# Kernel optimization log

Hardware: AMD Instinct MI355X
Metric: run time of the kernel (lower is better)

## Reference

```python
import jax, jax.numpy as jnp
import numpy as np

N_HEADS = 16
ROPE_BASE = 10000.0


def _rope_cos_sin(seq_len, head_dim, dtype):
    half = head_dim // 2
    inv_freq = 1.0 / (ROPE_BASE ** (jnp.arange(0, half, dtype=jnp.float32) / half))
    ang = jnp.arange(seq_len, dtype=jnp.float32)[:, None] * inv_freq[None, :]  # [S, half]
    cos = jnp.concatenate([jnp.cos(ang), jnp.cos(ang)], axis=-1).astype(dtype)  # [S, hd]
    sin = jnp.concatenate([jnp.sin(ang), jnp.sin(ang)], axis=-1).astype(dtype)
    return cos, sin


def _rotate_half(x):
    half = x.shape[-1] // 2
    return jnp.concatenate([-x[..., half:], x[..., :half]], axis=-1)


def setup_inputs() -> dict:
    key = jax.random.key(0)
    k1, k2, k3 = jax.random.split(key, 3)
    B, S, D = 2, 2048, 1024
    x = jax.random.normal(k1, (B, S, D), dtype=jnp.float32)
    w_qkv = jax.random.normal(k2, (D, 3 * D), dtype=jnp.float32) * (1.0 / np.sqrt(D))
    w_out = jax.random.normal(k3, (D, D), dtype=jnp.float32) * (1.0 / np.sqrt(D))
    return {"x": x, "w_qkv": w_qkv, "w_out": w_out}


def reference(x, w_qkv, w_out):
    B, S, D = x.shape
    H = N_HEADS
    hd = D // H
    scale = 1.0 / np.sqrt(hd)

    qkv = x @ w_qkv  # [B, S, 3D]
    q, k, v = jnp.split(qkv, 3, axis=-1)
    # [B, H, S, hd]
    q = q.reshape(B, S, H, hd).transpose(0, 2, 1, 3)
    k = k.reshape(B, S, H, hd).transpose(0, 2, 1, 3)
    v = v.reshape(B, S, H, hd).transpose(0, 2, 1, 3)

    cos, sin = _rope_cos_sin(S, hd, x.dtype)  # [S, hd]
    q = q * cos + _rotate_half(q) * sin
    k = k * cos + _rotate_half(k) * sin

    scores = jnp.einsum("bhqd,bhkd->bhqk", q, k) * scale  # [B, H, S, S]
    causal = jnp.tril(jnp.ones((S, S), dtype=bool))
    scores = jnp.where(causal[None, None, :, :], scores, -jnp.inf)

    probs = jax.nn.softmax(scores.astype(jnp.float32), axis=-1).astype(q.dtype)
    out = jnp.einsum("bhqk,bhkd->bhqd", probs, v)  # [B, H, S, hd]
    out = out.transpose(0, 2, 1, 3).reshape(B, S, D)
    return out @ w_out
```

## Files before the change

kernel.cpp:

```cpp
#include <hip/hip_runtime.h>
#include <math.h>
#include <type_traits>

#define B_  2
#define S_  2048
#define D_  1024
#define H_  16

typedef short bf16x8 __attribute__((ext_vector_type(8)));
typedef float f32x4  __attribute__((ext_vector_type(4)));

__device__ __forceinline__ short f2bf(float f) {
    unsigned u = __builtin_bit_cast(unsigned, f);
    u += 0x7FFFu + ((u >> 16) & 1u);
    return (short)(u >> 16);
}
__device__ __forceinline__ float bf2f(short s) {
    unsigned u = ((unsigned)(unsigned short)s) << 16;
    return __builtin_bit_cast(float, u);
}

__device__ __forceinline__ void gload16(const short* g, const void* l) {
    __builtin_amdgcn_global_load_lds(
        (const __attribute__((address_space(1))) void*)g,
        (__attribute__((address_space(3))) void*)l, 16, 0, 0);
}

__global__ __launch_bounds__(256) void cvt_bf16_kernel(
    const float* __restrict__ in, short* __restrict__ out)
{
    int i = (blockIdx.x * 256 + threadIdx.x) * 8;
    float4 a = *(const float4*)(in + i);
    float4 b = *(const float4*)(in + i + 4);
    bf16x8 o;
    o[0] = f2bf(a.x); o[1] = f2bf(a.y); o[2] = f2bf(a.z); o[3] = f2bf(a.w);
    o[4] = f2bf(b.x); o[5] = f2bf(b.y); o[6] = f2bf(b.z); o[7] = f2bf(b.w);
    *(bf16x8*)(out + i) = o;
}

__global__ __launch_bounds__(256) void transpose_cvt_kernel(
    const float* __restrict__ in, short* __restrict__ out, int K, int N)
{
    __shared__ short t[64][72];
    const int k0 = blockIdx.y * 64, n0 = blockIdx.x * 64;
    const int r = threadIdx.x >> 2;
    const int c = (threadIdx.x & 3) * 16;
    const float* src = in + (size_t)(k0 + r) * N + n0 + c;
#pragma unroll
    for (int i = 0; i < 16; ++i) t[c + i][r] = f2bf(src[i]);
    __syncthreads();
    short* dst = out + (size_t)(n0 + r) * K + k0 + c;
    *(bf16x8*)(dst)     = *(const bf16x8*)&t[r][c];
    *(bf16x8*)(dst + 8) = *(const bf16x8*)&t[r][c + 8];
}

__global__ __launch_bounds__(256) void rope_tab_kernel(float2* __restrict__ tab)
{
    int idx = blockIdx.x * 256 + threadIdx.x;
    int j = idx & 31, s = idx >> 5;
    float inv = powf(10000.0f, -(float)j * (1.0f / 32.0f));
    float sn, cs;
    sincosf((float)s * inv, &sn, &cs);
    tab[idx] = make_float2(cs, sn);
}

template <typename OutT>
__global__ __launch_bounds__(256) void gemm_bt(
    const short* __restrict__ A, const short* __restrict__ Bt,
    OutT* __restrict__ C, int M, int N, int K)
{
    __shared__ short As[128 * 32];
    __shared__ short Bs[128 * 32];

    const int tid  = threadIdx.x;
    const int wave = tid >> 6, lane = tid & 63;
    const int quad = lane >> 4, l16 = lane & 15;
    const int wm = wave >> 1, wn = wave & 1;
    const int row0 = blockIdx.y * 128, col0 = blockIdx.x * 128;

    f32x4 acc[4][4];
#pragma unroll
    for (int mi = 0; mi < 4; ++mi)
#pragma unroll
        for (int ni = 0; ni < 4; ++ni) acc[mi][ni] = (f32x4)0.f;

    const int sr = tid >> 2;
    const int sc = (tid & 3) * 8;
    const short* a0 = A  + (size_t)(row0 + sr) * K + sc;
    const short* a1 = A  + (size_t)(row0 + 64 + sr) * K + sc;
    const short* b0 = Bt + (size_t)(col0 + sr) * K + sc;
    const short* b1 = Bt + (size_t)(col0 + 64 + sr) * K + sc;
    char* lA0 = (char*)As + wave * 1024;
    char* lA1 = (char*)As + 4096 + wave * 1024;
    char* lB0 = (char*)Bs + wave * 1024;
    char* lB1 = (char*)Bs + 4096 + wave * 1024;

    for (int k0 = 0; k0 < K; k0 += 32) {
        __syncthreads();
        gload16(a0 + k0, lA0);
        gload16(a1 + k0, lA1);
        gload16(b0 + k0, lB0);
        gload16(b1 + k0, lB1);
        __syncthreads();

        bf16x8 af[4], bfr[4];
#pragma unroll
        for (int mi = 0; mi < 4; ++mi)
            af[mi] = *(const bf16x8*)(As + (wm * 64 + mi * 16 + l16) * 32 + quad * 8);
#pragma unroll
        for (int ni = 0; ni < 4; ++ni)
            bfr[ni] = *(const bf16x8*)(Bs + (wn * 64 + ni * 16 + l16) * 32 + quad * 8);
#pragma unroll
        for (int mi = 0; mi < 4; ++mi)
#pragma unroll
            for (int ni = 0; ni < 4; ++ni)
                acc[mi][ni] = __builtin_amdgcn_mfma_f32_16x16x32_bf16(
                    af[mi], bfr[ni], acc[mi][ni], 0, 0, 0);
    }

#pragma unroll
    for (int mi = 0; mi < 4; ++mi) {
#pragma unroll
        for (int ni = 0; ni < 4; ++ni) {
#pragma unroll
            for (int r = 0; r < 4; ++r) {
                int row = row0 + wm * 64 + mi * 16 + quad * 4 + r;
                int col = col0 + wn * 64 + ni * 16 + l16;
                float v = acc[mi][ni][r];
                if constexpr (std::is_same_v<OutT, short>)
                    C[(size_t)row * N + col] = f2bf(v);
                else
                    C[(size_t)row * N + col] = v;
            }
        }
    }
}

__global__ __launch_bounds__(256) void convert_kernel(
    const short* __restrict__ qkvb, const float2* __restrict__ tab,
    short* __restrict__ Qb, short* __restrict__ Kb, short* __restrict__ Vt)
{
    __shared__ short vtile[64][72];
    const int bh = blockIdx.y;
    const int st = blockIdx.x;
    const int b = bh >> 4, h = bh & 15;

    const int sl = threadIdx.x >> 2;
    const int g  = threadIdx.x & 3;
    const int s  = st * 64 + sl;
    const short* row = qkvb + (size_t)(b * S_ + s) * 3072 + h * 64;

    const int j0 = g * 8;
    bf16x8 q1v = *(const bf16x8*)(row + j0);
    bf16x8 q2v = *(const bf16x8*)(row + 32 + j0);
    bf16x8 k1v = *(const bf16x8*)(row + 1024 + j0);
    bf16x8 k2v = *(const bf16x8*)(row + 1056 + j0);
    bf16x8 qlo, qhi, klo, khi;
#pragma unroll
    for (int i = 0; i < 8; ++i) {
        float2 t = tab[s * 32 + j0 + i];
        float q1 = bf2f(q1v[i]), q2 = bf2f(q2v[i]);
        float k1 = bf2f(k1v[i]), k2 = bf2f(k2v[i]);
        qlo[i] = f2bf((q1 * t.x - q2 * t.y) * 0.125f);
        qhi[i] = f2bf((q2 * t.x + q1 * t.y) * 0.125f);
        klo[i] = f2bf(k1 * t.x - k2 * t.y);
        khi[i] = f2bf(k2 * t.x + k1 * t.y);
    }
    size_t oq = ((size_t)bh * S_ + s) * 64;
    *(bf16x8*)(Qb + oq + j0)      = qlo;
    *(bf16x8*)(Qb + oq + 32 + j0) = qhi;
    size_t ok = ((size_t)bh * S_ + s) * 72;
    *(bf16x8*)(Kb + ok + j0)      = klo;
    *(bf16x8*)(Kb + ok + 32 + j0) = khi;

    bf16x8 v0 = *(const bf16x8*)(row + 2048 + g * 16);
    bf16x8 v1 = *(const bf16x8*)(row + 2048 + g * 16 + 8);
#pragma unroll
    for (int i = 0; i < 8; ++i) {
        vtile[g * 16 + i][sl]     = v0[i];
        vtile[g * 16 + 8 + i][sl] = v1[i];
    }
    __syncthreads();
    size_t vo = ((size_t)bh * 64 + sl) * S_ + st * 64 + g * 16;
    *(bf16x8*)(Vt + vo)     = *(const bf16x8*)&vtile[sl][g * 16];
    *(bf16x8*)(Vt + vo + 8) = *(const bf16x8*)&vtile[sl][g * 16 + 8];
}

__global__ __launch_bounds__(256) void attn_kernel(
    const short* __restrict__ Qb, const short* __restrict__ Kb,
    const short* __restrict__ Vt, short* __restrict__ Opart,
    float* __restrict__ lpart)
{
    __shared__ short Ks[2][64 * 72];
    __shared__ short Vs[2][64 * 72];
    __shared__ short Ps[64][72];

    const int lin = blockIdx.x;
    const int xcd = lin & 7;
    const int j   = lin >> 3;
    const int bh   = xcd * 4 + (j & 3);
    const int task = j >> 2;

    const int g = task < 8 ? 0 : task < 24 ? 1 : task < 48 ? 2 : 3;
    const int cumstart = g == 0 ? 0 : g == 1 ? 8 : g == 2 ? 24 : 48;
    const int idx = task - cumstart;
    const int qd = idx / (g + 1);
    const int qb = 8 * g + qd;
    const int c  = idx - qd * (g + 1);
    const int t0 = c * 8;
    const int t1 = min(qb, c * 8 + 7);

    const int wave = threadIdx.x >> 6, lane = threadIdx.x & 63;
    const int quad = lane >> 4, l16 = lane & 15;
    const size_t head64 = (size_t)bh * S_ * 64;
    const size_t headK  = (size_t)bh * S_ * 72;

    const short* qrow = Qb + head64
        + (size_t)(qb * 64 + wave * 16 + l16) * 64 + quad * 8;
    const bf16x8 qf0 = *(const bf16x8*)(qrow);
    const bf16x8 qf1 = *(const bf16x8*)(qrow + 32);

    bf16x8 ones;
#pragma unroll
    for (int i = 0; i < 8; ++i) ones[i] = (short)0x3F80;

    int vr[3], vc[3];
#pragma unroll
    for (int u = 0; u < 3; ++u) {
        int jj = wave + u * 4;
        int e = jj * 64 + lane;
        vr[u] = e / 9;
        vc[u] = e * 8 - vr[u] * 72;
    }

    auto stageKV = [&](int buf, int t) {
        const short* kt  = Kb + headK + (size_t)t * 4608;
        const short* vtb = Vt + head64 + t * 64;
        short* kl = Ks[buf];
        short* vl = Vs[buf];
#pragma unroll
        for (int u = 0; u < 3; ++u) {
            int jj = wave + u * 4;
            if (jj < 9) {
                gload16(kt + jj * 512 + lane * 8, (char*)kl + jj * 1024);
                gload16(vtb + (size_t)vr[u] * S_ + vc[u], (char*)vl + jj * 1024);
            }
        }
    };

    f32x4 lacc = (f32x4)0.f;
    f32x4 oacc[4];
#pragma unroll
    for (int nt = 0; nt < 4; ++nt) oacc[nt] = (f32x4)0.f;

    int buf = 0;
    stageKV(0, t0);
    for (int t = t0; t <= t1; ++t) {
        __syncthreads();
        if (t < t1) stageKV(buf ^ 1, t + 1);

        const short* kb = Ks[buf];
        const short* vb = Vs[buf];

        f32x4 s4[4];
#pragma unroll
        for (int nt = 0; nt < 4; ++nt) {
            const short* kr = kb + (nt * 16 + l16) * 72 + quad * 8;
            bf16x8 b0 = *(const bf16x8*)kr;
            bf16x8 b1 = *(const bf16x8*)(kr + 32);
            f32x4 a = (f32x4)0.f;
            a = __builtin_amdgcn_mfma_f32_16x16x32_bf16(qf0, b0, a, 0, 0, 0);
            a = __builtin_amdgcn_mfma_f32_16x16x32_bf16(qf1, b1, a, 0, 0, 0);
            s4[nt] = a;
        }

        if (t == qb) {
#pragma unroll
            for (int nt = 0; nt < 4; ++nt)
#pragma unroll
                for (int r = 0; r < 4; ++r)
                    if (nt * 16 + l16 > wave * 16 + quad * 4 + r)
                        s4[nt][r] = -INFINITY;
        }

#pragma unroll
        for (int nt = 0; nt < 4; ++nt)
#pragma unroll
            for (int r = 0; r < 4; ++r)
                Ps[wave * 16 + quad * 4 + r][nt * 16 + l16] =
                    f2bf(__expf(s4[nt][r] - 8.0f));

        bf16x8 pa0 = *(const bf16x8*)&Ps[wave * 16 + l16][quad * 8];
        bf16x8 pa1 = *(const bf16x8*)&Ps[wave * 16 + l16][32 + quad * 8];
        lacc = __builtin_amdgcn_mfma_f32_16x16x32_bf16(pa0, ones, lacc, 0, 0, 0);
        lacc = __builtin_amdgcn_mfma_f32_16x16x32_bf16(pa1, ones, lacc, 0, 0, 0);
#pragma unroll
        for (int nt = 0; nt < 4; ++nt) {
            const short* vrp = vb + (nt * 16 + l16) * 72 + quad * 8;
            bf16x8 vb0 = *(const bf16x8*)vrp;
            bf16x8 vb1 = *(const bf16x8*)(vrp + 32);
            oacc[nt] = __builtin_amdgcn_mfma_f32_16x16x32_bf16(
                pa0, vb0, oacc[nt], 0, 0, 0);
            oacc[nt] = __builtin_amdgcn_mfma_f32_16x16x32_bf16(
                pa1, vb1, oacc[nt], 0, 0, 0);
        }
        buf ^= 1;
    }

    const int pidx = bh * 80 + task;
#pragma unroll
    for (int r = 0; r < 4; ++r) {
        int ql = wave * 16 + quad * 4 + r;
        short* orow = Opart + (size_t)pidx * 4096 + ql * 64;
#pragma unroll
        for (int nt = 0; nt < 4; ++nt)
            orow[nt * 16 + l16] = f2bf(oacc[nt][r]);
        if (l16 == 0)
            lpart[(size_t)pidx * 64 + ql] = lacc[r];
    }
}

__global__ __launch_bounds__(256) void combine_kernel(
    const short* __restrict__ Opart, const float* __restrict__ lpart,
    short* __restrict__ attnb)
{
    const int qb = blockIdx.x, bh = blockIdx.y;
    const int g = qb >> 3, nch = g + 1;
    const int cbase = bh * 80 + nch * (qb - 4 * g);
    const int q = threadIdx.x >> 2;
    const int dg = (threadIdx.x & 3) * 16;

    float lsum = 0.f;
    float acc[16];
#pragma unroll
    for (int i = 0; i < 16; ++i) acc[i] = 0.f;

    for (int cc = 0; cc < nch; ++cc) {
        lsum += lpart[(size_t)(cbase + cc) * 64 + q];
        const short* src = Opart + (size_t)(cbase + cc) * 4096 + q * 64 + dg;
        bf16x8 o0 = *(const bf16x8*)src;
        bf16x8 o1 = *(const bf16x8*)(src + 8);
#pragma unroll
        for (int i = 0; i < 8; ++i) {
            acc[i]     += bf2f(o0[i]);
            acc[i + 8] += bf2f(o1[i]);
        }
    }
    float inv = 1.0f / lsum;
    const int b = bh >> 4, h = bh & 15;
    bf16x8 r0, r1;
#pragma unroll
    for (int i = 0; i < 8; ++i) {
        r0[i] = f2bf(acc[i] * inv);
        r1[i] = f2bf(acc[i + 8] * inv);
    }
    short* dst = attnb + (size_t)(b * S_ + qb * 64 + q) * 1024 + h * 64 + dg;
    *(bf16x8*)dst       = r0;
    *(bf16x8*)(dst + 8) = r1;
}

extern "C" void kernel_launch(void* const* d_in, const int* in_sizes, int n_in,
                              void* d_out, int out_size, void* d_ws, size_t ws_size,
                              hipStream_t stream)
{
    const float* x     = (const float*)d_in[0];
    const float* w_qkv = (const float*)d_in[1];
    const float* w_out = (const float*)d_in[2];
    float* out = (float*)d_out;

    short* qkvb = (short*)d_ws;
    short* Qb   = qkvb + (size_t)4096 * 3072;
    short* Kb   = Qb   + (size_t)4096 * 1024;
    short* Vt   = Kb   + (size_t)32 * 2048 * 72;
    short* Xb   = Vt   + (size_t)4096 * 1024;
    short* Wqt  = Xb   + (size_t)4096 * 1024;
    short* Wot  = Wqt  + (size_t)3072 * 1024;
    float2* tab = (float2*)(Wot + (size_t)1024 * 1024);
    short* Opart = qkvb;
    float* lbuf  = (float*)Wqt;
    short* attnb = Xb;

    cvt_bf16_kernel<<<(4096 * 1024 / 8) / 256, 256, 0, stream>>>(x, Xb);
    transpose_cvt_kernel<<<dim3(3072 / 64, 1024 / 64), 256, 0, stream>>>(
        w_qkv, Wqt, 1024, 3072);
    transpose_cvt_kernel<<<dim3(1024 / 64, 1024 / 64), 256, 0, stream>>>(
        w_out, Wot, 1024, 1024);
    rope_tab_kernel<<<(2048 * 32) / 256, 256, 0, stream>>>(tab);

    gemm_bt<short><<<dim3(3072 / 128, 4096 / 128), 256, 0, stream>>>(
        Xb, Wqt, qkvb, 4096, 3072, 1024);

    convert_kernel<<<dim3(S_ / 64, B_ * H_), 256, 0, stream>>>(qkvb, tab, Qb, Kb, Vt);

    attn_kernel<<<2560, 256, 0, stream>>>(Qb, Kb, Vt, Opart, lbuf);

    combine_kernel<<<dim3(32, 32), 256, 0, stream>>>(Opart, lbuf, attnb);

    gemm_bt<float><<<dim3(1024 / 128, 4096 / 128), 256, 0, stream>>>(
        attnb, Wot, out, 4096, 1024, 1024);
}
```

Baseline: 210.7 us.

## Double attention query tile to 128 rows per block for K/V reuse

Each attention block now handles 128 query rows (two 16-row MFMA subtiles per wave) instead of 64, so every staged K/V tile in LDS feeds twice as many MFMAs. The grid halves to 1280 blocks, the split-KV task map is rebuilt for 128-row query tiles, the causal mask uses absolute positions, and combine_kernel reads the new partial layout. This cuts global K/V traffic and LDS staging per unit of work, at the cost of more registers, a larger LDS P buffer, fewer blocks, and some wasted masked work on diagonal tiles.

```diff
diff --git a/kernel.cpp b/kernel.cpp
--- a/kernel.cpp
+++ b/kernel.cpp
@@ -193,32 +193,34 @@
 {
     __shared__ short Ks[2][64 * 72];
     __shared__ short Vs[2][64 * 72];
-    __shared__ short Ps[64][72];
+    __shared__ short Ps[128][72];
 
     const int lin = blockIdx.x;
     const int xcd = lin & 7;
-    const int j   = lin >> 3;
-    const int bh   = xcd * 4 + (j & 3);
-    const int task = j >> 2;
-
-    const int g = task < 8 ? 0 : task < 24 ? 1 : task < 48 ? 2 : 3;
-    const int cumstart = g == 0 ? 0 : g == 1 ? 8 : g == 2 ? 24 : 48;
-    const int idx = task - cumstart;
-    const int qd = idx / (g + 1);
-    const int qb = 8 * g + qd;
-    const int c  = idx - qd * (g + 1);
+    const int bh   = xcd * 4 + ((lin >> 3) & 3);
+    const int task = lin >> 5;
+
+    const int g = task < 4 ? 0 : task < 12 ? 1 : task < 24 ? 2 : 3;
+    const int cum = g == 0 ? 0 : g == 1 ? 4 : g == 2 ? 12 : 24;
+    const int idx = task - cum;
+    const int qt = 4 * g + idx / (g + 1);
+    const int c  = idx % (g + 1);
     const int t0 = c * 8;
-    const int t1 = min(qb, c * 8 + 7);
+    const int t1 = min(2 * qt + 1, c * 8 + 7);
 
     const int wave = threadIdx.x >> 6, lane = threadIdx.x & 63;
     const int quad = lane >> 4, l16 = lane & 15;
     const size_t head64 = (size_t)bh * S_ * 64;
     const size_t headK  = (size_t)bh * S_ * 72;
 
-    const short* qrow = Qb + head64
-        + (size_t)(qb * 64 + wave * 16 + l16) * 64 + quad * 8;
-    const bf16x8 qf0 = *(const bf16x8*)(qrow);
-    const bf16x8 qf1 = *(const bf16x8*)(qrow + 32);
+    bf16x8 qf[2][2];
+#pragma unroll
+    for (int mi = 0; mi < 2; ++mi) {
+        const short* qrow = Qb + head64
+            + (size_t)(qt * 128 + wave * 32 + mi * 16 + l16) * 64 + quad * 8;
+        qf[mi][0] = *(const bf16x8*)(qrow);
+        qf[mi][1] = *(const bf16x8*)(qrow + 32);
+    }
 
     bf16x8 ones;
 #pragma unroll
@@ -248,10 +250,14 @@
         }
     };
 
-    f32x4 lacc = (f32x4)0.f;
-    f32x4 oacc[4];
-#pragma unroll
-    for (int nt = 0; nt < 4; ++nt) oacc[nt] = (f32x4)0.f;
+    f32x4 lacc[2];
+    f32x4 oacc[2][4];
+#pragma unroll
+    for (int mi = 0; mi < 2; ++mi) {
+        lacc[mi] = (f32x4)0.f;
+#pragma unroll
+        for (int nt = 0; nt < 4; ++nt) oacc[mi][nt] = (f32x4)0.f;
+    }
 
     int buf = 0;
     stageKV(0, t0);
@@ -262,62 +268,81 @@
         const short* kb = Ks[buf];
         const short* vb = Vs[buf];
 
-        f32x4 s4[4];
+        f32x4 s4[2][4];
 #pragma unroll
         for (int nt = 0; nt < 4; ++nt) {
             const short* kr = kb + (nt * 16 + l16) * 72 + quad * 8;
             bf16x8 b0 = *(const bf16x8*)kr;
             bf16x8 b1 = *(const bf16x8*)(kr + 32);
-            f32x4 a = (f32x4)0.f;
-            a = __builtin_amdgcn_mfma_f32_16x16x32_bf16(qf0, b0, a, 0, 0, 0);
-            a = __builtin_amdgcn_mfma_f32_16x16x32_bf16(qf1, b1, a, 0, 0, 0);
-            s4[nt] = a;
-        }
-
-        if (t == qb) {
+#pragma unroll
+            for (int mi = 0; mi < 2; ++mi) {
+                f32x4 a = (f32x4)0.f;
+                a = __builtin_amdgcn_mfma_f32_16x16x32_bf16(qf[mi][0], b0, a, 0, 0, 0);
+                a = __builtin_amdgcn_mfma_f32_16x16x32_bf16(qf[mi][1], b1, a, 0, 0, 0);
+                s4[mi][nt] = a;
+            }
+        }
+
+        if (t >= 2 * qt) {
+            const int kbase = t * 64;
+            const int qbase = qt * 128 + wave * 32 + quad * 4;
+#pragma unroll
+            for (int mi = 0; mi < 2; ++mi)
+#pragma unroll
+                for (int nt = 0; nt < 4; ++nt)
+#pragma unroll
+                    for (int r = 0; r < 4; ++r)
+                        if (kbase + nt * 16 + l16 > qbase + mi * 16 + r)
+                            s4[mi][nt][r] = -INFINITY;
+        }
+
+#pragma unroll
+        for (int mi = 0; mi < 2; ++mi)
 #pragma unroll
             for (int nt = 0; nt < 4; ++nt)
 #pragma unroll
                 for (int r = 0; r < 4; ++r)
-                    if (nt * 16 + l16 > wave * 16 + quad * 4 + r)
-                        s4[nt][r] = -INFINITY;
-        }
-
-#pragma unroll
-        for (int nt = 0; nt < 4; ++nt)
-#pragma unroll
-            for (int r = 0; r < 4; ++r)
-                Ps[wave * 16 + quad * 4 + r][nt * 16 + l16] =
-                    f2bf(__expf(s4[nt][r] - 8.0f));
-
-        bf16x8 pa0 = *(const bf16x8*)&Ps[wave * 16 + l16][quad * 8];
-        bf16x8 pa1 = *(const bf16x8*)&Ps[wave * 16 + l16][32 + quad * 8];
-        lacc = __builtin_amdgcn_mfma_f32_16x16x32_bf16(pa0, ones, lacc, 0, 0, 0);
-        lacc = __builtin_amdgcn_mfma_f32_16x16x32_bf16(pa1, ones, lacc, 0, 0, 0);
+                    Ps[wave * 32 + mi * 16 + quad * 4 + r][nt * 16 + l16] =
+                        f2bf(__expf(s4[mi][nt][r] - 8.0f));
+
+        bf16x8 vfr[4][2];
 #pragma unroll
         for (int nt = 0; nt < 4; ++nt) {
             const short* vrp = vb + (nt * 16 + l16) * 72 + quad * 8;
-            bf16x8 vb0 = *(const bf16x8*)vrp;
-            bf16x8 vb1 = *(const bf16x8*)(vrp + 32);
-            oacc[nt] = __builtin_amdgcn_mfma_f32_16x16x32_bf16(
-                pa0, vb0, oacc[nt], 0, 0, 0);
-            oacc[nt] = __builtin_amdgcn_mfma_f32_16x16x32_bf16(
-                pa1, vb1, oacc[nt], 0, 0, 0);
+            vfr[nt][0] = *(const bf16x8*)vrp;
+            vfr[nt][1] = *(const bf16x8*)(vrp + 32);
+        }
+
+#pragma unroll
+        for (int mi = 0; mi < 2; ++mi) {
+            bf16x8 pa0 = *(const bf16x8*)&Ps[wave * 32 + mi * 16 + l16][quad * 8];
+            bf16x8 pa1 = *(const bf16x8*)&Ps[wave * 32 + mi * 16 + l16][32 + quad * 8];
+            lacc[mi] = __builtin_amdgcn_mfma_f32_16x16x32_bf16(pa0, ones, lacc[mi], 0, 0, 0);
+            lacc[mi] = __builtin_amdgcn_mfma_f32_16x16x32_bf16(pa1, ones, lacc[mi], 0, 0, 0);
+#pragma unroll
+            for (int nt = 0; nt < 4; ++nt) {
+                oacc[mi][nt] = __builtin_amdgcn_mfma_f32_16x16x32_bf16(
+                    pa0, vfr[nt][0], oacc[mi][nt], 0, 0, 0);
+                oacc[mi][nt] = __builtin_amdgcn_mfma_f32_16x16x32_bf16(
+                    pa1, vfr[nt][1], oacc[mi][nt], 0, 0, 0);
+            }
         }
         buf ^= 1;
     }
 
-    const int pidx = bh * 80 + task;
-#pragma unroll
-    for (int r = 0; r < 4; ++r) {
-        int ql = wave * 16 + quad * 4 + r;
-        short* orow = Opart + (size_t)pidx * 4096 + ql * 64;
-#pragma unroll
-        for (int nt = 0; nt < 4; ++nt)
-            orow[nt * 16 + l16] = f2bf(oacc[nt][r]);
-        if (l16 == 0)
-            lpart[(size_t)pidx * 64 + ql] = lacc[r];
-    }
+    const int pidx = bh * 40 + task;
+#pragma unroll
+    for (int mi = 0; mi < 2; ++mi)
+#pragma unroll
+        for (int r = 0; r < 4; ++r) {
+            int ql = wave * 32 + mi * 16 + quad * 4 + r;
+            short* orow = Opart + (size_t)pidx * 8192 + ql * 64;
+#pragma unroll
+            for (int nt = 0; nt < 4; ++nt)
+                orow[nt * 16 + l16] = f2bf(oacc[mi][nt][r]);
+            if (l16 == 0)
+                lpart[(size_t)pidx * 128 + ql] = lacc[mi][r];
+        }
 }
 
 __global__ __launch_bounds__(256) void combine_kernel(
@@ -325,10 +350,15 @@
     short* __restrict__ attnb)
 {
     const int qb = blockIdx.x, bh = blockIdx.y;
-    const int g = qb >> 3, nch = g + 1;
-    const int cbase = bh * 80 + nch * (qb - 4 * g);
+    const int qt = qb >> 1;
+    const int g = qt < 4 ? 0 : qt < 8 ? 1 : qt < 12 ? 2 : 3;
+    const int tb = (g == 0 ? 0 : g == 1 ? 4 : g == 2 ? 12 : 24)
+                   + (qt - 4 * g) * (g + 1);
+    const int nch = g + 1;
+    const int cbase = bh * 40 + tb;
     const int q = threadIdx.x >> 2;
     const int dg = (threadIdx.x & 3) * 16;
+    const int qrow = (qb & 1) * 64 + q;
 
     float lsum = 0.f;
     float acc[16];
@@ -336,8 +366,8 @@
     for (int i = 0; i < 16; ++i) acc[i] = 0.f;
 
     for (int cc = 0; cc < nch; ++cc) {
-        lsum += lpart[(size_t)(cbase + cc) * 64 + q];
-        const short* src = Opart + (size_t)(cbase + cc) * 4096 + q * 64 + dg;
+        lsum += lpart[(size_t)(cbase + cc) * 128 + qrow];
+        const short* src = Opart + (size_t)(cbase + cc) * 8192 + qrow * 64 + dg;
         bf16x8 o0 = *(const bf16x8*)src;
         bf16x8 o1 = *(const bf16x8*)(src + 8);
 #pragma unroll
@@ -392,7 +422,7 @@
 
     convert_kernel<<<dim3(S_ / 64, B_ * H_), 256, 0, stream>>>(qkvb, tab, Qb, Kb, Vt);
 
-    attn_kernel<<<2560, 256, 0, stream>>>(Qb, Kb, Vt, Opart, lbuf);
+    attn_kernel<<<1280, 256, 0, stream>>>(Qb, Kb, Vt, Opart, lbuf);
 
     combine_kernel<<<dim3(32, 32), 256, 0, stream>>>(Opart, lbuf, attnb);
 
```

After: 209.8 us. Within noise of the previous version (-0.4%).

## Fuse RoPE, scaling and V transpose into QKV GEMM epilogue

Applied to the files above, without the earlier changes.

The separate convert kernel is removed. The QKV GEMM epilogue now applies RoPE and the Q scale and writes Q/K in head-major layout, and it writes V transposed directly. This saves the round trip of the bf16 qkv intermediate through global memory and one kernel launch. In exchange, the epilogue stores are scalar 2-byte writes, or 8-byte writes for V, with strided addresses. The workspace is re-laid out so Opart and lbuf no longer alias the old qkv buffer.

```diff
diff --git a/kernel.cpp b/kernel.cpp
--- a/kernel.cpp
+++ b/kernel.cpp
@@ -8,6 +8,7 @@
 #define H_  16
 
 typedef short bf16x8 __attribute__((ext_vector_type(8)));
+typedef short bf16x4 __attribute__((ext_vector_type(4)));
 typedef float f32x4  __attribute__((ext_vector_type(4)));
 
 __device__ __forceinline__ short f2bf(float f) {
@@ -64,10 +65,9 @@
     tab[idx] = make_float2(cs, sn);
 }
 
-template <typename OutT>
-__global__ __launch_bounds__(256) void gemm_bt(
+__global__ __launch_bounds__(256) void gemm_bt_f32(
     const short* __restrict__ A, const short* __restrict__ Bt,
-    OutT* __restrict__ C, int M, int N, int K)
+    float* __restrict__ C, int M, int N, int K)
 {
     __shared__ short As[128 * 32];
     __shared__ short Bs[128 * 32];
@@ -119,71 +119,121 @@
     }
 
 #pragma unroll
-    for (int mi = 0; mi < 4; ++mi) {
-#pragma unroll
-        for (int ni = 0; ni < 4; ++ni) {
+    for (int mi = 0; mi < 4; ++mi)
+#pragma unroll
+        for (int ni = 0; ni < 4; ++ni)
 #pragma unroll
             for (int r = 0; r < 4; ++r) {
                 int row = row0 + wm * 64 + mi * 16 + quad * 4 + r;
                 int col = col0 + wn * 64 + ni * 16 + l16;
-                float v = acc[mi][ni][r];
-                if constexpr (std::is_same_v<OutT, short>)
-                    C[(size_t)row * N + col] = f2bf(v);
-                else
-                    C[(size_t)row * N + col] = v;
+                C[(size_t)row * N + col] = acc[mi][ni][r];
             }
-        }
-    }
-}
-
-__global__ __launch_bounds__(256) void convert_kernel(
-    const short* __restrict__ qkvb, const float2* __restrict__ tab,
+}
+
+__global__ __launch_bounds__(256) void gemm_qkv(
+    const short* __restrict__ A, const short* __restrict__ Bt,
+    const float2* __restrict__ tab,
     short* __restrict__ Qb, short* __restrict__ Kb, short* __restrict__ Vt)
 {
-    __shared__ short vtile[64][72];
-    const int bh = blockIdx.y;
-    const int st = blockIdx.x;
-    const int b = bh >> 4, h = bh & 15;
-
-    const int sl = threadIdx.x >> 2;
-    const int g  = threadIdx.x & 3;
-    const int s  = st * 64 + sl;
-    const short* row = qkvb + (size_t)(b * S_ + s) * 3072 + h * 64;
-
-    const int j0 = g * 8;
-    bf16x8 q1v = *(const bf16x8*)(row + j0);
-    bf16x8 q2v = *(const bf16x8*)(row + 32 + j0);
-    bf16x8 k1v = *(const bf16x8*)(row + 1024 + j0);
-    bf16x8 k2v = *(const bf16x8*)(row + 1056 + j0);
-    bf16x8 qlo, qhi, klo, khi;
-#pragma unroll
-    for (int i = 0; i < 8; ++i) {
-        float2 t = tab[s * 32 + j0 + i];
-        float q1 = bf2f(q1v[i]), q2 = bf2f(q2v[i]);
-        float k1 = bf2f(k1v[i]), k2 = bf2f(k2v[i]);
-        qlo[i] = f2bf((q1 * t.x - q2 * t.y) * 0.125f);
-        qhi[i] = f2bf((q2 * t.x + q1 * t.y) * 0.125f);
-        klo[i] = f2bf(k1 * t.x - k2 * t.y);
-        khi[i] = f2bf(k2 * t.x + k1 * t.y);
-    }
-    size_t oq = ((size_t)bh * S_ + s) * 64;
-    *(bf16x8*)(Qb + oq + j0)      = qlo;
-    *(bf16x8*)(Qb + oq + 32 + j0) = qhi;
-    size_t ok = ((size_t)bh * S_ + s) * 72;
-    *(bf16x8*)(Kb + ok + j0)      = klo;
-    *(bf16x8*)(Kb + ok + 32 + j0) = khi;
-
-    bf16x8 v0 = *(const bf16x8*)(row + 2048 + g * 16);
-    bf16x8 v1 = *(const bf16x8*)(row + 2048 + g * 16 + 8);
-#pragma unroll
-    for (int i = 0; i < 8; ++i) {
-        vtile[g * 16 + i][sl]     = v0[i];
-        vtile[g * 16 + 8 + i][sl] = v1[i];
-    }
-    __syncthreads();
-    size_t vo = ((size_t)bh * 64 + sl) * S_ + st * 64 + g * 16;
-    *(bf16x8*)(Vt + vo)     = *(const bf16x8*)&vtile[sl][g * 16];
-    *(bf16x8*)(Vt + vo + 8) = *(const bf16x8*)&vtile[sl][g * 16 + 8];
+    const int K = 1024;
+    __shared__ short As[128 * 32];
+    __shared__ short Bs[128 * 32];
+
+    const int tid  = threadIdx.x;
+    const int wave = tid >> 6, lane = tid & 63;
+    const int quad = lane >> 4, l16 = lane & 15;
+    const int wm = wave >> 1, wn = wave & 1;
+    const int row0 = blockIdx.y * 128, col0 = blockIdx.x * 128;
+
+    f32x4 acc[4][4];
+#pragma unroll
+    for (int mi = 0; mi < 4; ++mi)
+#pragma unroll
+        for (int ni = 0; ni < 4; ++ni) acc[mi][ni] = (f32x4)0.f;
+
+    const int sr = tid >> 2;
+    const int sc = (tid & 3) * 8;
+    const short* a0 = A  + (size_t)(row0 + sr) * K + sc;
+    const short* a1 = A  + (size_t)(row0 + 64 + sr) * K + sc;
+    const short* b0 = Bt + (size_t)(col0 + sr) * K + sc;
+    const short* b1 = Bt + (size_t)(col0 + 64 + sr) * K + sc;
+    char* lA0 = (char*)As + wave * 1024;
+    char* lA1 = (char*)As + 4096 + wave * 1024;
+    char* lB0 = (char*)Bs + wave * 1024;
+    char* lB1 = (char*)Bs + 4096 + wave * 1024;
+
+    for (int k0 = 0; k0 < K; k0 += 32) {
+        __syncthreads();
+        gload16(a0 + k0, lA0);
+        gload16(a1 + k0, lA1);
+        gload16(b0 + k0, lB0);
+        gload16(b1 + k0, lB1);
+        __syncthreads();
+
+        bf16x8 af[4], bfr[4];
+#pragma unroll
+        for (int mi = 0; mi < 4; ++mi)
+            af[mi] = *(const bf16x8*)(As + (wm * 64 + mi * 16 + l16) * 32 + quad * 8);
+#pragma unroll
+        for (int ni = 0; ni < 4; ++ni)
+            bfr[ni] = *(const bf16x8*)(Bs + (wn * 64 + ni * 16 + l16) * 32 + quad * 8);
+#pragma unroll
+        for (int mi = 0; mi < 4; ++mi)
+#pragma unroll
+            for (int ni = 0; ni < 4; ++ni)
+                acc[mi][ni] = __builtin_amdgcn_mfma_f32_16x16x32_bf16(
+                    af[mi], bfr[ni], acc[mi][ni], 0, 0, 0);
+    }
+
+    const int sec  = (col0 + wn * 64) >> 6;
+    const int h    = sec & 15;
+    const int kind = sec >> 4;
+
+    if (kind < 2) {
+#pragma unroll
+        for (int mi = 0; mi < 4; ++mi) {
+#pragma unroll
+            for (int r = 0; r < 4; ++r) {
+                int row = row0 + wm * 64 + mi * 16 + quad * 4 + r;
+                int b = row >> 11, s = row & (S_ - 1);
+                int bh = b * 16 + h;
+#pragma unroll
+                for (int ni = 0; ni < 2; ++ni) {
+                    int j = ni * 16 + l16;
+                    float2 t = tab[s * 32 + j];
+                    float lo = acc[mi][ni][r], hi = acc[mi][ni + 2][r];
+                    float olo = lo * t.x - hi * t.y;
+                    float ohi = hi * t.x + lo * t.y;
+                    if (kind == 0) {
+                        size_t base = ((size_t)bh * S_ + s) * 64;
+                        Qb[base + j]      = f2bf(olo * 0.125f);
+                        Qb[base + 32 + j] = f2bf(ohi * 0.125f);
+                    } else {
+                        size_t base = ((size_t)bh * S_ + s) * 72;
+                        Kb[base + j]      = f2bf(olo);
+                        Kb[base + 32 + j] = f2bf(ohi);
+                    }
+                }
+            }
+        }
+    } else {
+#pragma unroll
+        for (int mi = 0; mi < 4; ++mi) {
+            int srow0 = row0 + wm * 64 + mi * 16 + quad * 4;
+            int b = srow0 >> 11, s0 = srow0 & (S_ - 1);
+            int bh = b * 16 + h;
+#pragma unroll
+            for (int ni = 0; ni < 4; ++ni) {
+                int d = ni * 16 + l16;
+                bf16x4 p;
+                p[0] = f2bf(acc[mi][ni][0]);
+                p[1] = f2bf(acc[mi][ni][1]);
+                p[2] = f2bf(acc[mi][ni][2]);
+                p[3] = f2bf(acc[mi][ni][3]);
+                *(bf16x4*)(Vt + ((size_t)bh * 64 + d) * S_ + s0) = p;
+            }
+        }
+    }
 }
 
 __global__ __launch_bounds__(256) void attn_kernel(
@@ -368,16 +418,15 @@
     const float* w_out = (const float*)d_in[2];
     float* out = (float*)d_out;
 
-    short* qkvb = (short*)d_ws;
-    short* Qb   = qkvb + (size_t)4096 * 3072;
+    short* Qb   = (short*)d_ws;
     short* Kb   = Qb   + (size_t)4096 * 1024;
     short* Vt   = Kb   + (size_t)32 * 2048 * 72;
     short* Xb   = Vt   + (size_t)4096 * 1024;
     short* Wqt  = Xb   + (size_t)4096 * 1024;
     short* Wot  = Wqt  + (size_t)3072 * 1024;
     float2* tab = (float2*)(Wot + (size_t)1024 * 1024);
-    short* Opart = qkvb;
-    float* lbuf  = (float*)Wqt;
+    short* Opart = (short*)(tab + 2048 * 32);
+    float* lbuf  = (float*)(Opart + (size_t)2560 * 4096);
     short* attnb = Xb;
 
     cvt_bf16_kernel<<<(4096 * 1024 / 8) / 256, 256, 0, stream>>>(x, Xb);
@@ -387,15 +436,13 @@
         w_out, Wot, 1024, 1024);
     rope_tab_kernel<<<(2048 * 32) / 256, 256, 0, stream>>>(tab);
 
-    gemm_bt<short><<<dim3(3072 / 128, 4096 / 128), 256, 0, stream>>>(
-        Xb, Wqt, qkvb, 4096, 3072, 1024);
-
-    convert_kernel<<<dim3(S_ / 64, B_ * H_), 256, 0, stream>>>(qkvb, tab, Qb, Kb, Vt);
+    gemm_qkv<<<dim3(3072 / 128, 4096 / 128), 256, 0, stream>>>(
+        Xb, Wqt, tab, Qb, Kb, Vt);
 
     attn_kernel<<<2560, 256, 0, stream>>>(Qb, Kb, Vt, Opart, lbuf);
 
     combine_kernel<<<dim3(32, 32), 256, 0, stream>>>(Opart, lbuf, attnb);
 
-    gemm_bt<float><<<dim3(1024 / 128, 4096 / 128), 256, 0, stream>>>(
+    gemm_bt_f32<<<dim3(1024 / 128, 4096 / 128), 256, 0, stream>>>(
         attnb, Wot, out, 4096, 1024, 1024);
 }
```

Result: slower. 226.4 us (+7.4%).
